# Kernel tuning notes

Hardware: AMD Instinct MI355X
Metric: run time of the kernel (lower is better)

## Reference

```python
import jax, jax.numpy as jnp
import numpy as np


def _ln(x, g, b, eps=1e-5):
    m = x.mean(-1, keepdims=True)
    v = x.var(-1, keepdims=True)
    return (x - m) / jnp.sqrt(v + eps) * g + b


def setup_inputs() -> dict:
    key = jax.random.key(0)
    ks = iter(jax.random.split(key, 48))
    B, N, H, Ld, L, FF = 2048, 10, 256, 8, 4, 1024
    def w(shape, s=0.02):
        return jax.random.normal(next(ks), shape, jnp.float32) * s
    return dict(
        latent_code=jax.random.normal(next(ks), (B, Ld), jnp.float32),
        target_node_types=jax.random.randint(next(ks), (B, N), 0, 5),
        ce_w1=w((Ld, H)), ce_b1=jnp.zeros(H), ce_g1=jnp.ones(H), ce_be1=jnp.zeros(H),
        ce_w2=w((H, H)), ce_b2=jnp.zeros(H), ce_g2=jnp.ones(H), ce_be2=jnp.zeros(H),
        nc_w1=w((2, H // 4)), nc_b1=jnp.zeros(H // 4), nc_w2=w((H // 4, 3)), nc_b2=jnp.zeros(3),
        type_emb=w((5, H), 1.0), pos_emb=w((N, H), 0.02),
        qkvo_w=w((L, 4, H, H)), qkvo_b=jnp.zeros((L, 4, H)),
        ln_g=jnp.ones((L, 2, H)), ln_b=jnp.zeros((L, 2, H)),
        ffn_w1=w((L, H, FF)), ffn_b1=jnp.zeros((L, FF)),
        ffn_w2=w((L, FF, H)), ffn_b2=jnp.zeros((L, H)),
        out_w=w((H, 5)), out_b=jnp.zeros(5),
        edge_w1=w((2 * H + Ld, H)), edge_b1=jnp.zeros(H),
        edge_w2=w((H, 8)), edge_b2=jnp.zeros(8),
    )


def reference(latent_code, target_node_types,
              ce_w1, ce_b1, ce_g1, ce_be1, ce_w2, ce_b2, ce_g2, ce_be2,
              nc_w1, nc_b1, nc_w2, nc_b2,
              type_emb, pos_emb, qkvo_w, qkvo_b, ln_g, ln_b,
              ffn_w1, ffn_b1, ffn_w2, ffn_b2, out_w, out_b,
              edge_w1, edge_b1, edge_w2, edge_b2):
    B, Ld = latent_code.shape
    N = target_node_types.shape[1]
    H = ce_w1.shape[1]
    L = qkvo_w.shape[0]
    nh = 8
    hd = H // nh

    # context encoder: Linear -> LN -> ReLU -> Linear -> LN
    h0 = jax.nn.relu(_ln(latent_code @ ce_w1 + ce_b1, ce_g1, ce_be1))
    context = _ln(h0 @ ce_w2 + ce_b2, ce_g2, ce_be2)  # [B,H]

    # node count head on latent_code[:, :2]
    node_count_logits = jax.nn.relu(latent_code[:, :2] @ nc_w1 + nc_b1) @ nc_w2 + nc_b2  # [B,3]

    # teacher-forced node embeddings (independent of predictions -> vectorizable)
    ne = type_emb[target_node_types] + pos_emb[:N]          # [B,N,H]
    h = context[:, None, :] + pos_emb[:N]                   # queries [B,N,H]
    mem = jnp.concatenate([context[:, None, :], ne], axis=1)  # keys [B,N+1,H]
    # position i attends to context (k=0) and nodes j<i (k=j+1), i.e. k <= i
    kmask = (jnp.arange(N + 1)[None, :] <= jnp.arange(N)[:, None])  # [N,N+1]
    scale = 1.0 / np.sqrt(hd).astype(np.float32)

    for l in range(L):
        Q = (h @ qkvo_w[l, 0] + qkvo_b[l, 0]).reshape(B, N, nh, hd)
        K = (mem @ qkvo_w[l, 1] + qkvo_b[l, 1]).reshape(B, N + 1, nh, hd)
        V = (mem @ qkvo_w[l, 2] + qkvo_b[l, 2]).reshape(B, N + 1, nh, hd)
        s = jnp.einsum('bnhd,bmhd->bhnm', Q, K) * scale
        s = jnp.where(kmask[None, None], s, jnp.float32(-1e9))
        a = jax.nn.softmax(s, axis=-1)
        o = jnp.einsum('bhnm,bmhd->bnhd', a, V).reshape(B, N, H)
        h = _ln(h + o @ qkvo_w[l, 3] + qkvo_b[l, 3], ln_g[l, 0], ln_b[l, 0])
        f = jax.nn.relu(h @ ffn_w1[l] + ffn_b1[l]) @ ffn_w2[l] + ffn_b2[l]
        h = _ln(h + f, ln_g[l, 1], ln_b[l, 1])

    node_logits = h @ out_w + out_b  # [B,N,5]

    # pairwise edge decoder on (emb_i, emb_j, latent) for i>j, symmetrized
    ei = jnp.broadcast_to(ne[:, :, None, :], (B, N, N, H))
    ej = jnp.broadcast_to(ne[:, None, :, :], (B, N, N, H))
    lat = jnp.broadcast_to(latent_code[:, None, None, :], (B, N, N, Ld))
    feat = jnp.concatenate([ei, ej, lat], axis=-1)  # [B,N,N,2H+Ld]
    elog = jax.nn.relu(feat @ edge_w1 + edge_b1) @ edge_w2 + edge_b2  # [B,N,N,8]
    tril = (jnp.arange(N)[:, None] > jnp.arange(N)[None, :])[None, :, :, None]
    lower = jnp.where(tril, elog, jnp.float32(0.0))
    edge_component_logits = lower + jnp.swapaxes(lower, 1, 2)  # diag stays zero

    return node_logits, node_count_logits, edge_component_logits
```

## Files before the change

kernel.cpp:

```cpp
#include <hip/hip_runtime.h>
#include <hip/hip_bf16.h>

#define BATCH 2048
#define NNODE 10
#define NLAYER 4
#define ROWS_H (BATCH*NNODE)
#define ROWS_M (BATCH*(NNODE+1))

typedef __hip_bfloat16 bf16;
typedef unsigned short u16;
typedef unsigned int u32;
typedef __attribute__((ext_vector_type(8))) short bf16x8;
typedef __attribute__((ext_vector_type(4))) float f32x4;

__device__ __forceinline__ float bfb(u16 u) {
    union { u32 i; float f; } c; c.i = (u32)u << 16; return c.f;
}
__device__ __forceinline__ float bf2f(bf16 x) { return __bfloat162float(x); }
__device__ __forceinline__ bf16 f2bf(float x) { return __float2bfloat16(x); }
__device__ __forceinline__ u16 f2u(float v) {
    bf16 t = f2bf(v); u16 u; __builtin_memcpy(&u, &t, 2); return u;
}
__device__ __forceinline__ void store_out(void* out, int f32o, size_t idx, float v) {
    if (f32o) ((float*)out)[idx] = v; else ((bf16*)out)[idx] = f2bf(v);
}
__device__ __forceinline__ int dflag(const u32* g) { return g[0] == 0x3F800000u; }

#define NT 26
struct CvtArgs { const void* src[NT]; int n[NT]; int off[NT]; };

__global__ __launch_bounds__(256) void cvt_kernel(CvtArgs a, bf16* __restrict__ dst,
                                                  const u32* __restrict__ gptr) {
    int f = dflag(gptr);
    int gid = blockIdx.x * 256 + threadIdx.x;
    int stride = gridDim.x * 256;
    for (int tn = 0; tn < NT; tn++) {
        const void* s = a.src[tn];
        bf16* d = dst + a.off[tn];
        int n = a.n[tn];
        if (f) {
            const float* sf = (const float*)s;
            for (int i = gid; i < n; i += stride) d[i] = f2bf(sf[i]);
        } else {
            const bf16* sb = (const bf16*)s;
            for (int i = gid; i < n; i += stride) d[i] = sb[i];
        }
    }
}

#define NTT 26
struct TTArgs { const void* src[NTT]; int soff[NTT]; int doff[NTT]; int R[NTT]; int Cc[NTT]; };

__global__ __launch_bounds__(256) void tt_kernel(TTArgs a, u16* __restrict__ dst,
                                                 const u32* __restrict__ gptr) {
    int f = dflag(gptr);
    int gid = blockIdx.x * 256 + threadIdx.x;
    int stride = gridDim.x * 256;
    for (int tn = 0; tn < NTT; tn++) {
        int R = a.R[tn], C = a.Cc[tn], n = R * C;
        u16* d = dst + a.doff[tn];
        if (f) {
            const float* s = (const float*)a.src[tn] + a.soff[tn];
            for (int i = gid; i < n; i += stride) {
                int r = i / C, c = i - r * C;
                d[c * R + r] = f2u(s[i]);
            }
        } else {
            const u16* s = (const u16*)a.src[tn] + a.soff[tn];
            for (int i = gid; i < n; i += stride) {
                int r = i / C, c = i - r * C;
                d[c * R + r] = s[i];
            }
        }
    }
}

__device__ __forceinline__ void ln_stats256(float x, float* s_red, float& m, float& var) {
    float v1 = x, v2 = x * x;
    #pragma unroll
    for (int off = 32; off; off >>= 1) {
        v1 += __shfl_down(v1, off, 64);
        v2 += __shfl_down(v2, off, 64);
    }
    int wave = threadIdx.x >> 6, lane = threadIdx.x & 63;
    if (!lane) { s_red[wave] = v1; s_red[4 + wave] = v2; }
    __syncthreads();
    m   = (s_red[0] + s_red[1] + s_red[2] + s_red[3]) * (1.f / 256.f);
    var = (s_red[4] + s_red[5] + s_red[6] + s_red[7]) * (1.f / 256.f) - m * m;
    __syncthreads();
}

__global__ __launch_bounds__(256) void ctx_kernel(
    const bf16* __restrict__ lat_bf, const int* __restrict__ types,
    const bf16* __restrict__ ce_w1, const bf16* __restrict__ ce_b1,
    const bf16* __restrict__ ce_g1, const bf16* __restrict__ ce_be1,
    const bf16* __restrict__ ce_w2, const bf16* __restrict__ ce_b2,
    const bf16* __restrict__ ce_g2, const bf16* __restrict__ ce_be2,
    const bf16* __restrict__ nc_w1, const bf16* __restrict__ nc_b1,
    const bf16* __restrict__ nc_w2, const bf16* __restrict__ nc_b2,
    const bf16* __restrict__ type_emb, const bf16* __restrict__ pos_emb,
    const bf16* __restrict__ edge_w1, const bf16* __restrict__ edge_b1,
    bf16* __restrict__ h, bf16* __restrict__ mem, bf16* __restrict__ ne,
    bf16* __restrict__ rvec, void* __restrict__ out, const u32* __restrict__ gptr)
{
    int b = blockIdx.x;
    int t = threadIdx.x;
    int f32o = dflag(gptr);
    __shared__ float lat[8];
    __shared__ float s_h0[256];
    __shared__ float s_red[8];
    __shared__ float s_nc[64];

    if (t < 8) lat[t] = bf2f(lat_bf[b * 8 + t]);
    __syncthreads();

    float x = bf2f(ce_b1[t]);
    #pragma unroll
    for (int k = 0; k < 8; k++) x += lat[k] * bf2f(ce_w1[k * 256 + t]);
    float m, var;
    ln_stats256(x, s_red, m, var);
    float r = rsqrtf(var + 1e-5f);
    float h0 = fmaxf((x - m) * r * bf2f(ce_g1[t]) + bf2f(ce_be1[t]), 0.f);
    s_h0[t] = h0;
    __syncthreads();

    float x2 = bf2f(ce_b2[t]);
    for (int k = 0; k < 256; k++) x2 += s_h0[k] * bf2f(ce_w2[k * 256 + t]);
    ln_stats256(x2, s_red, m, var);
    r = rsqrtf(var + 1e-5f);
    float ctx = (x2 - m) * r * bf2f(ce_g2[t]) + bf2f(ce_be2[t]);

    mem[(size_t)(b * 11) * 256 + t] = f2bf(ctx);
    for (int n = 0; n < NNODE; n++) {
        float pe = bf2f(pos_emb[n * 256 + t]);
        h[(size_t)(b * NNODE + n) * 256 + t] = f2bf(ctx + pe);
        int ty = types[b * NNODE + n];
        float nv = bf2f(type_emb[ty * 256 + t]) + pe;
        ne[(size_t)(b * NNODE + n) * 256 + t] = f2bf(nv);
        mem[(size_t)(b * 11 + 1 + n) * 256 + t] = f2bf(nv);
    }

    float rv = bf2f(edge_b1[t]);
    #pragma unroll
    for (int k = 0; k < 8; k++) rv += lat[k] * bf2f(edge_w1[(512 + k) * 256 + t]);
    rvec[(size_t)b * 256 + t] = f2bf(rv);

    if (t < 64) {
        float hn = lat[0] * bf2f(nc_w1[t]) + lat[1] * bf2f(nc_w1[64 + t]) + bf2f(nc_b1[t]);
        s_nc[t] = fmaxf(hn, 0.f);
    }
    __syncthreads();
    if (t < 3) {
        float o = bf2f(nc_b2[t]);
        for (int k = 0; k < 64; k++) o += s_nc[k] * bf2f(nc_w2[k * 3 + t]);
        store_out(out, f32o, (size_t)102400 + b * 3 + t, o);
    }
}

__global__ __launch_bounds__(256) void gemm_mfma(
    const u16* __restrict__ A, const u16* __restrict__ Bt,
    const bf16* __restrict__ bias, bf16* __restrict__ C,
    int M, int K, int N, int act)
{
    __shared__ u16 Als[128 * 32];
    __shared__ u16 Bls[128 * 32];
    int t = threadIdx.x;
    int w = t >> 6, l = t & 63;
    int m0 = blockIdx.y * 128, n0 = blockIdx.x * 128;
    int wr = (w >> 1) * 64, wc = (w & 1) * 64;

    int srow = w * 32 + (l >> 2);
    int selem = (l & 3) * 8;
    const u16* Ag = A + (size_t)(m0 + srow) * K + selem;
    const u16* Bg = Bt + (size_t)(n0 + srow) * K + selem;

    f32x4 acc[4][4];
    #pragma unroll
    for (int i = 0; i < 4; i++)
        #pragma unroll
        for (int j = 0; j < 4; j++)
            acc[i][j] = (f32x4){0.f, 0.f, 0.f, 0.f};

    int koff = (l >> 4) * 8;
    int mrow = wr + (l & 15);
    int ncol = wc + (l & 15);

    for (int kt = 0; kt < K; kt += 32) {
        const u16* ag = Ag + kt;
        const u16* bg = Bg + kt;
        __builtin_amdgcn_global_load_lds(
            (const __attribute__((address_space(1))) void*)ag,
            (__attribute__((address_space(3))) void*)&Als[w * 1024], 16, 0, 0);
        __builtin_amdgcn_global_load_lds(
            (const __attribute__((address_space(1))) void*)(ag + (size_t)16 * K),
            (__attribute__((address_space(3))) void*)&Als[w * 1024 + 512], 16, 0, 0);
        __builtin_amdgcn_global_load_lds(
            (const __attribute__((address_space(1))) void*)bg,
            (__attribute__((address_space(3))) void*)&Bls[w * 1024], 16, 0, 0);
        __builtin_amdgcn_global_load_lds(
            (const __attribute__((address_space(1))) void*)(bg + (size_t)16 * K),
            (__attribute__((address_space(3))) void*)&Bls[w * 1024 + 512], 16, 0, 0);
        __syncthreads();

        bf16x8 af[4], bfr[4];
        #pragma unroll
        for (int i = 0; i < 4; i++) {
            af[i]  = *(const bf16x8*)&Als[(mrow + i * 16) * 32 + koff];
            bfr[i] = *(const bf16x8*)&Bls[(ncol + i * 16) * 32 + koff];
        }
        #pragma unroll
        for (int i = 0; i < 4; i++)
            #pragma unroll
            for (int j = 0; j < 4; j++)
                acc[i][j] = __builtin_amdgcn_mfma_f32_16x16x32_bf16(af[i], bfr[j], acc[i][j], 0, 0, 0);
        __syncthreads();
    }

    int rbase = (l >> 4) * 4;
    #pragma unroll
    for (int i = 0; i < 4; i++) {
        int m = m0 + wr + i * 16 + rbase;
        #pragma unroll
        for (int j = 0; j < 4; j++) {
            int n = n0 + wc + j * 16 + (l & 15);
            float bv = bias ? bf2f(bias[n]) : 0.f;
            #pragma unroll
            for (int r = 0; r < 4; r++) {
                float v = acc[i][j][r] + bv;
                if (act) v = fmaxf(v, 0.f);
                C[(size_t)(m + r) * N + n] = f2bf(v);
            }
        }
    }
}

template<int MODE>
__global__ __launch_bounds__(256) void gemm_row(
    const u16* __restrict__ A, const u16* __restrict__ Bt,
    const bf16* __restrict__ bias, const bf16* __restrict__ g,
    const bf16* __restrict__ be, u16* __restrict__ hio,
    u16* __restrict__ C, int M, int K)
{
    __shared__ u16 Als[64 * 32];
    __shared__ u16 Bls[256 * 32];
    __shared__ float s_bias[256], s_g[256], s_be[256];
    int t = threadIdx.x;
    int w = t >> 6, l = t & 63;
    int m0 = blockIdx.x * 64;

    s_bias[t] = bf2f(bias[t]);
    if (MODE == 1) { s_g[t] = bf2f(g[t]); s_be[t] = bf2f(be[t]); }

    int srow = l >> 2, selem = (l & 3) * 8;
    const u16* Ag = A + (size_t)(m0 + w * 16 + srow) * K + selem;
    const u16* Bg = Bt + (size_t)(w * 64 + srow) * K + selem;

    f32x4 acc[16];
    #pragma unroll
    for (int j = 0; j < 16; j++) acc[j] = (f32x4){0.f, 0.f, 0.f, 0.f};

    int koff = (l >> 4) * 8;
    int l15 = l & 15;

    for (int kt = 0; kt < K; kt += 32) {
        __builtin_amdgcn_global_load_lds(
            (const __attribute__((address_space(1))) void*)(Ag + kt),
            (__attribute__((address_space(3))) void*)&Als[w * 512], 16, 0, 0);
        #pragma unroll
        for (int s = 0; s < 4; s++) {
            __builtin_amdgcn_global_load_lds(
                (const __attribute__((address_space(1))) void*)(Bg + kt + (size_t)(s * 16) * K),
                (__attribute__((address_space(3))) void*)&Bls[w * 2048 + s * 512], 16, 0, 0);
        }
        __syncthreads();

        bf16x8 af = *(const bf16x8*)&Als[(w * 16 + l15) * 32 + koff];
        #pragma unroll
        for (int j = 0; j < 16; j++) {
            bf16x8 bf = *(const bf16x8*)&Bls[(j * 16 + l15) * 32 + koff];
            acc[j] = __builtin_amdgcn_mfma_f32_16x16x32_bf16(af, bf, acc[j], 0, 0, 0);
        }
        __syncthreads();
    }

    int q = l >> 4;
    #pragma unroll
    for (int r = 0; r < 4; r++) {
        int row = m0 + w * 16 + q * 4 + r;
        if (MODE == 0) {
            #pragma unroll
            for (int j = 0; j < 16; j++) {
                int col = j * 16 + l15;
                C[(size_t)row * 256 + col] = f2u(acc[j][r] + s_bias[col]);
            }
        } else {
            float xs[16];
            float s = 0.f, s2 = 0.f;
            #pragma unroll
            for (int j = 0; j < 16; j++) {
                int col = j * 16 + l15;
                float xv = acc[j][r] + s_bias[col] + bfb(hio[(size_t)row * 256 + col]);
                xs[j] = xv; s += xv; s2 += xv * xv;
            }
            #pragma unroll
            for (int off = 8; off; off >>= 1) {
                s  += __shfl_xor(s, off, 64);
                s2 += __shfl_xor(s2, off, 64);
            }
            float mean = s * (1.f / 256.f);
            float var = s2 * (1.f / 256.f) - mean * mean;
            float rstd = rsqrtf(var + 1e-5f);
            #pragma unroll
            for (int j = 0; j < 16; j++) {
                int col = j * 16 + l15;
                hio[(size_t)row * 256 + col] = f2u((xs[j] - mean) * rstd * s_g[col] + s_be[col]);
            }
        }
    }
}

__global__ __launch_bounds__(256) void attn_kernel(
    const bf16* __restrict__ Qb, const bf16* __restrict__ KVb,
    bf16* __restrict__ Ob)
{
    int b = blockIdx.x;
    int t = threadIdx.x;
    __shared__ float Qs[10 * 256];
    __shared__ float Ks[11 * 256];
    __shared__ float S[880];

    for (int i = 0; i < 10; i++) Qs[i * 256 + t] = bf2f(Qb[(size_t)(b * 10 + i) * 256 + t]);
    for (int k = 0; k < 11; k++) Ks[k * 256 + t] = bf2f(KVb[(size_t)(b * 11 + k) * 512 + t]);
    __syncthreads();

    const float scale = 0.17677669529663687f;
    for (int e = t; e < 880; e += 256) {
        int head = e / 110, rem = e % 110, i = rem / 11, k = rem % 11;
        if (k <= i) {
            const float* qp = &Qs[i * 256 + head * 32];
            const float* kp = &Ks[k * 256 + head * 32];
            float s = 0.f;
            #pragma unroll
            for (int d = 0; d < 32; d++) s += qp[d] * kp[d];
            S[e] = s * scale;
        }
    }
    __syncthreads();
    if (t < 80) {
        int head = t / 10, i = t % 10;
        float* row = &S[head * 110 + i * 11];
        float mx = -1e30f;
        for (int k = 0; k <= i; k++) mx = fmaxf(mx, row[k]);
        float sum = 0.f;
        for (int k = 0; k <= i; k++) { float e = __expf(row[k] - mx); row[k] = e; sum += e; }
        float inv = 1.f / sum;
        for (int k = 0; k <= i; k++) row[k] *= inv;
    }
    __syncthreads();

    int head = t >> 5;
    float o[10] = {0.f, 0.f, 0.f, 0.f, 0.f, 0.f, 0.f, 0.f, 0.f, 0.f};
    for (int k = 0; k < 11; k++) {
        float v = bf2f(KVb[(size_t)(b * 11 + k) * 512 + 256 + t]);
        for (int i = k; i < 10; i++) o[i] += S[head * 110 + i * 11 + k] * v;
    }
    for (int i = 0; i < 10; i++) Ob[(size_t)(b * 10 + i) * 256 + t] = f2bf(o[i]);
}

__global__ __launch_bounds__(256) void outhead_kernel(
    const bf16* __restrict__ h, const bf16* __restrict__ w,
    const bf16* __restrict__ b, void* __restrict__ out, const u32* __restrict__ gptr)
{
    int f32o = dflag(gptr);
    int wv = threadIdx.x >> 6, l = threadIdx.x & 63;
    size_t row = (size_t)blockIdx.x * 4 + wv;
    ushort4 hv = *(const ushort4*)((const u16*)h + row * 256 + l * 4);
    float x[4] = {bfb(hv.x), bfb(hv.y), bfb(hv.z), bfb(hv.w)};
    float a[5] = {0.f, 0.f, 0.f, 0.f, 0.f};
    #pragma unroll
    for (int c = 0; c < 4; c++) {
        #pragma unroll
        for (int o = 0; o < 5; o++) a[o] += x[c] * bf2f(w[(l * 4 + c) * 5 + o]);
    }
    #pragma unroll
    for (int off = 32; off; off >>= 1)
        #pragma unroll
        for (int o = 0; o < 5; o++) a[o] += __shfl_xor(a[o], off, 64);
    if (!l)
        #pragma unroll
        for (int o = 0; o < 5; o++)
            store_out(out, f32o, row * 5 + o, a[o] + bf2f(b[o]));
}

__global__ __launch_bounds__(256) void edge_kernel(
    const bf16* __restrict__ PQ, const bf16* __restrict__ rvec,
    const bf16* __restrict__ w2, const bf16* __restrict__ b2,
    void* __restrict__ out, const u32* __restrict__ gptr)
{
    int f32o = dflag(gptr);
    int t = threadIdx.x, w = t >> 6, l = t & 63;
    int b = blockIdx.x * 4 + w;
    const size_t ebase = 108544;

    __shared__ u16 Pl[4][10 * 260];
    __shared__ u16 Ql[4][10 * 260];
    __shared__ u16 Rl[4][256];
    __shared__ float Wl[256 * 8];

    const u16* pq = (const u16*)PQ + (size_t)b * 10 * 512;
    #pragma unroll
    for (int i = 0; i < 10; i++) {
        ushort4 pv = *(const ushort4*)(pq + i * 512 + l * 4);
        ushort4 qv = *(const ushort4*)(pq + i * 512 + 256 + l * 4);
        *(ushort4*)&Pl[w][i * 260 + l * 4] = pv;
        *(ushort4*)&Ql[w][i * 260 + l * 4] = qv;
    }
    *(ushort4*)&Rl[w][l * 4] = *(const ushort4*)((const u16*)rvec + (size_t)b * 256 + l * 4);
    {
        const u16* wp = (const u16*)w2 + t * 8;
        #pragma unroll
        for (int o = 0; o < 8; o++) Wl[t * 8 + o] = bfb(wp[o]);
    }
    __syncthreads();

    if (l >= 45 && l < 55) {
        int i = l - 45;
        size_t o0 = ebase + ((size_t)(b * 10 + i) * 10 + i) * 8;
        if (f32o) {
            float4 z = {0.f, 0.f, 0.f, 0.f};
            *(float4*)((float*)out + o0) = z;
            *(float4*)((float*)out + o0 + 4) = z;
        } else {
            uint4 z = {0u, 0u, 0u, 0u};
            *(uint4*)((u16*)out + o0) = z;
        }
    }
    if (l < 45) {
        int i = 1;
        while (i * (i + 1) / 2 <= l) i++;
        int j = l - i * (i - 1) / 2;
        float acc[8] = {0.f, 0.f, 0.f, 0.f, 0.f, 0.f, 0.f, 0.f};
        const u16* Pp = &Pl[w][i * 260];
        const u16* Qp = &Ql[w][j * 260];
        const u16* Rp = &Rl[w][0];
        for (int c = 0; c < 256; c += 4) {
            ushort4 pv = *(const ushort4*)(Pp + c);
            ushort4 qv = *(const ushort4*)(Qp + c);
            ushort4 rv = *(const ushort4*)(Rp + c);
            float hc[4];
            hc[0] = fmaxf(bfb(pv.x) + bfb(qv.x) + bfb(rv.x), 0.f);
            hc[1] = fmaxf(bfb(pv.y) + bfb(qv.y) + bfb(rv.y), 0.f);
            hc[2] = fmaxf(bfb(pv.z) + bfb(qv.z) + bfb(rv.z), 0.f);
            hc[3] = fmaxf(bfb(pv.w) + bfb(qv.w) + bfb(rv.w), 0.f);
            #pragma unroll
            for (int cc = 0; cc < 4; cc++) {
                const float* wp = &Wl[(c + cc) * 8];
                #pragma unroll
                for (int o = 0; o < 8; o++) acc[o] += hc[cc] * wp[o];
            }
        }
        float r8[8];
        #pragma unroll
        for (int o = 0; o < 8; o++) r8[o] = acc[o] + bf2f(b2[o]);
        size_t o0 = ebase + ((size_t)(b * 10 + i) * 10 + j) * 8;
        size_t o1 = ebase + ((size_t)(b * 10 + j) * 10 + i) * 8;
        if (f32o) {
            float4 v0 = {r8[0], r8[1], r8[2], r8[3]};
            float4 v1 = {r8[4], r8[5], r8[6], r8[7]};
            *(float4*)((float*)out + o0) = v0; *(float4*)((float*)out + o0 + 4) = v1;
            *(float4*)((float*)out + o1) = v0; *(float4*)((float*)out + o1 + 4) = v1;
        } else {
            uint4 pk;
            pk.x = (u32)f2u(r8[0]) | ((u32)f2u(r8[1]) << 16);
            pk.y = (u32)f2u(r8[2]) | ((u32)f2u(r8[3]) << 16);
            pk.z = (u32)f2u(r8[4]) | ((u32)f2u(r8[5]) << 16);
            pk.w = (u32)f2u(r8[6]) | ((u32)f2u(r8[7]) << 16);
            *(uint4*)((u16*)out + o0) = pk;
            *(uint4*)((u16*)out + o1) = pk;
        }
    }
}

extern "C" void kernel_launch(void* const* d_in, const int* in_sizes, int n_in,
                              void* d_out, int out_size, void* d_ws, size_t ws_size,
                              hipStream_t stream) {
    const int* types = (const int*)d_in[1];
    const u32* gptr = (const u32*)d_in[18];

    static const int kIdx[NT] = {0,2,3,4,5,6,7,8,9,10,11,12,13,14,15,17,18,19,21,23,24,25,26,27,28,29};
    static const int kSz[NT]  = {16384,2048,256,256,256,65536,256,256,256,128,64,192,3,1280,2560,
                                 4096,2048,2048,4096,1024,1280,5,133120,256,2048,8};
    bf16* wbf = (bf16*)d_ws;

    CvtArgs ca;
    const bf16* cv[30];
    int off = 0;
    for (int i = 0; i < NT; i++) {
        ca.src[i] = d_in[kIdx[i]];
        ca.n[i] = kSz[i];
        ca.off[i] = off;
        cv[kIdx[i]] = wbf + off;
        off = (off + kSz[i] + 7) & ~7;
    }

    size_t wtbase_e = ((size_t)off + 127) & ~(size_t)127;
    u16* wt = (u16*)wbf + wtbase_e;
    TTArgs ta;
    int tn = 0;
    for (int l = 0; l < NLAYER; l++) {
        int base = l * 786432;
        for (int z = 0; z < 4; z++) {
            static const int dz[4] = {0, 65536, 131072, 196608};
            ta.src[tn] = d_in[16]; ta.soff[tn] = (l * 4 + z) * 65536;
            ta.doff[tn] = base + dz[z]; ta.R[tn] = 256; ta.Cc[tn] = 256; tn++;
        }
        ta.src[tn] = d_in[20]; ta.soff[tn] = l * 262144; ta.doff[tn] = base + 262144; ta.R[tn] = 256;  ta.Cc[tn] = 1024; tn++;
        ta.src[tn] = d_in[22]; ta.soff[tn] = l * 262144; ta.doff[tn] = base + 524288; ta.R[tn] = 1024; ta.Cc[tn] = 256;  tn++;
    }
    ta.src[tn] = d_in[26]; ta.soff[tn] = 0;     ta.doff[tn] = 3145728;         ta.R[tn] = 256; ta.Cc[tn] = 256; tn++;
    ta.src[tn] = d_in[26]; ta.soff[tn] = 65536; ta.doff[tn] = 3145728 + 65536; ta.R[tn] = 256; ta.Cc[tn] = 256; tn++;

    size_t actbase_e = wtbase_e + 3276800 + 128;

    size_t EH = (size_t)ROWS_H * 256, EM = (size_t)ROWS_M * 256;
    bf16* p = (bf16*)wbf + actbase_e;
    bf16* h    = p; p += EH;
    bf16* mem  = p; p += EM;
    bf16* ne   = p; p += EH;
    bf16* rvec = p; p += (size_t)BATCH * 256;
    bf16* span = p;
    bf16* qbuf = span;
    bf16* kvbuf = qbuf + EH;
    bf16* obuf = kvbuf + (size_t)ROWS_M * 512;
    bf16* fbuf = span;
    bf16* pqbuf = span;

    cvt_kernel<<<256, 256, 0, stream>>>(ca, wbf, gptr);
    tt_kernel<<<512, 256, 0, stream>>>(ta, wt, gptr);

    ctx_kernel<<<BATCH, 256, 0, stream>>>(
        cv[0], types, cv[2], cv[3], cv[4], cv[5], cv[6], cv[7], cv[8], cv[9],
        cv[10], cv[11], cv[12], cv[13], cv[14], cv[15], cv[26], cv[27],
        h, mem, ne, rvec, d_out, gptr);

    for (int l = 0; l < NLAYER; l++) {
        const u16* qT  = wt + (size_t)l * 786432;
        const u16* kvT = qT + 65536;
        const u16* oT  = qT + 196608;
        const u16* f1T = qT + 262144;
        const u16* f2T = qT + 524288;
        const bf16* bq  = cv[17] + (size_t)(l * 4 + 0) * 256;
        const bf16* bkv = cv[17] + (size_t)(l * 4 + 1) * 256;
        const bf16* bo  = cv[17] + (size_t)(l * 4 + 3) * 256;
        const bf16* g1 = cv[18] + (size_t)(l * 2) * 256, *be1 = cv[19] + (size_t)(l * 2) * 256;
        const bf16* g2 = cv[18] + (size_t)(l * 2 + 1) * 256, *be2 = cv[19] + (size_t)(l * 2 + 1) * 256;

        gemm_row<0><<<ROWS_H / 64, 256, 0, stream>>>((const u16*)h, qT, bq, nullptr, nullptr,
                                                     nullptr, (u16*)qbuf, ROWS_H, 256);
        gemm_mfma<<<dim3(4, ROWS_M / 128), 256, 0, stream>>>((const u16*)mem, kvT, bkv, kvbuf, ROWS_M, 256, 512, 0);
        attn_kernel<<<BATCH, 256, 0, stream>>>(qbuf, kvbuf, obuf);
        gemm_row<1><<<ROWS_H / 64, 256, 0, stream>>>((const u16*)obuf, oT, bo, g1, be1,
                                                     (u16*)h, nullptr, ROWS_H, 256);
        gemm_mfma<<<dim3(8, ROWS_H / 128), 256, 0, stream>>>((const u16*)h, f1T, cv[21] + (size_t)l * 1024, fbuf, ROWS_H, 256, 1024, 1);
        gemm_row<1><<<ROWS_H / 64, 256, 0, stream>>>((const u16*)fbuf, f2T, cv[23] + (size_t)l * 256, g2, be2,
                                                     (u16*)h, nullptr, ROWS_H, 1024);
    }

    outhead_kernel<<<ROWS_H / 4, 256, 0, stream>>>(h, cv[24], cv[25], d_out, gptr);

    gemm_mfma<<<dim3(4, ROWS_H / 128), 256, 0, stream>>>((const u16*)ne, wt + 3145728, nullptr, pqbuf, ROWS_H, 256, 512, 0);
    edge_kernel<<<BATCH / 4, 256, 0, stream>>>(pqbuf, rvec, cv[28], cv[29], d_out, gptr);
}
```

Baseline: 743.2 us.

## Fuse FFN up/down projections into one kernel and retile row GEMMs

Replaces the separate FFN up-projection GEMM and down-projection+LayerNorm GEMM with a single kernel. Each 64-row block keeps its input rows and the ReLU intermediate in LDS, streaming 128-column chunks of the hidden layer so the 1024-wide intermediate never goes to global memory. It also retiles the 256-column row GEMM so each wave owns a 64-column slice across all 64 rows, with LayerNorm statistics reduced across waves through shared memory. The cost is more LDS per block, lower occupancy, and the FFN loops run serially inside one block with many syncs.

Result: no change. 738.9 us (-0.6%).

```diff
diff --git a/kernel.cpp b/kernel.cpp
--- a/kernel.cpp
+++ b/kernel.cpp
@@ -25,6 +25,10 @@
     if (f32o) ((float*)out)[idx] = v; else ((bf16*)out)[idx] = f2bf(v);
 }
 __device__ __forceinline__ int dflag(const u32* g) { return g[0] == 0x3F800000u; }
+
+#define GLL(src, dst) __builtin_amdgcn_global_load_lds( \
+    (const __attribute__((address_space(1))) void*)(src), \
+    (__attribute__((address_space(3))) void*)(dst), 16, 0, 0)
 
 #define NT 26
 struct CvtArgs { const void* src[NT]; int n[NT]; int off[NT]; };
@@ -188,18 +192,10 @@
     for (int kt = 0; kt < K; kt += 32) {
         const u16* ag = Ag + kt;
         const u16* bg = Bg + kt;
-        __builtin_amdgcn_global_load_lds(
-            (const __attribute__((address_space(1))) void*)ag,
-            (__attribute__((address_space(3))) void*)&Als[w * 1024], 16, 0, 0);
-        __builtin_amdgcn_global_load_lds(
-            (const __attribute__((address_space(1))) void*)(ag + (size_t)16 * K),
-            (__attribute__((address_space(3))) void*)&Als[w * 1024 + 512], 16, 0, 0);
-        __builtin_amdgcn_global_load_lds(
-            (const __attribute__((address_space(1))) void*)bg,
-            (__attribute__((address_space(3))) void*)&Bls[w * 1024], 16, 0, 0);
-        __builtin_amdgcn_global_load_lds(
-            (const __attribute__((address_space(1))) void*)(bg + (size_t)16 * K),
-            (__attribute__((address_space(3))) void*)&Bls[w * 1024 + 512], 16, 0, 0);
+        GLL(ag, &Als[w * 1024]);
+        GLL(ag + (size_t)16 * K, &Als[w * 1024 + 512]);
+        GLL(bg, &Bls[w * 1024]);
+        GLL(bg + (size_t)16 * K, &Bls[w * 1024 + 512]);
         __syncthreads();
 
         bf16x8 af[4], bfr[4];
@@ -235,88 +231,241 @@
 }
 
 template<int MODE>
-__global__ __launch_bounds__(256) void gemm_row(
+__global__ __launch_bounds__(256) void gemm256(
     const u16* __restrict__ A, const u16* __restrict__ Bt,
     const bf16* __restrict__ bias, const bf16* __restrict__ g,
     const bf16* __restrict__ be, u16* __restrict__ hio,
-    u16* __restrict__ C, int M, int K)
+    u16* __restrict__ C, int K)
 {
-    __shared__ u16 Als[64 * 32];
-    __shared__ u16 Bls[256 * 32];
-    __shared__ float s_bias[256], s_g[256], s_be[256];
-    int t = threadIdx.x;
-    int w = t >> 6, l = t & 63;
+    __shared__ u16 Asl[64 * 32];
+    __shared__ u16 Bsl[256 * 32];
+    __shared__ float lnp[2][4][64];
+    int t = threadIdx.x, w = t >> 6, l = t & 63, q = l >> 4, l15 = l & 15;
     int m0 = blockIdx.x * 64;
 
-    s_bias[t] = bf2f(bias[t]);
-    if (MODE == 1) { s_g[t] = bf2f(g[t]); s_be[t] = bf2f(be[t]); }
-
-    int srow = l >> 2, selem = (l & 3) * 8;
-    const u16* Ag = A + (size_t)(m0 + w * 16 + srow) * K + selem;
-    const u16* Bg = Bt + (size_t)(w * 64 + srow) * K + selem;
-
-    f32x4 acc[16];
-    #pragma unroll
-    for (int j = 0; j < 16; j++) acc[j] = (f32x4){0.f, 0.f, 0.f, 0.f};
-
-    int koff = (l >> 4) * 8;
-    int l15 = l & 15;
+    const u16* Ag = A + (size_t)(m0 + w * 16 + (l >> 2)) * K + (l & 3) * 8;
+    const u16* Bg = Bt + (size_t)(w * 64 + (l >> 2)) * K + (l & 3) * 8;
+
+    f32x4 acc[4][4];
+    #pragma unroll
+    for (int i = 0; i < 4; i++)
+        #pragma unroll
+        for (int j = 0; j < 4; j++)
+            acc[i][j] = (f32x4){0.f, 0.f, 0.f, 0.f};
 
     for (int kt = 0; kt < K; kt += 32) {
-        __builtin_amdgcn_global_load_lds(
-            (const __attribute__((address_space(1))) void*)(Ag + kt),
-            (__attribute__((address_space(3))) void*)&Als[w * 512], 16, 0, 0);
-        #pragma unroll
-        for (int s = 0; s < 4; s++) {
-            __builtin_amdgcn_global_load_lds(
-                (const __attribute__((address_space(1))) void*)(Bg + kt + (size_t)(s * 16) * K),
-                (__attribute__((address_space(3))) void*)&Bls[w * 2048 + s * 512], 16, 0, 0);
-        }
+        GLL(Ag + kt, &Asl[w * 512]);
+        #pragma unroll
+        for (int s = 0; s < 4; s++)
+            GLL(Bg + kt + (size_t)(s * 16) * K, &Bsl[w * 2048 + s * 512]);
         __syncthreads();
-
-        bf16x8 af = *(const bf16x8*)&Als[(w * 16 + l15) * 32 + koff];
-        #pragma unroll
-        for (int j = 0; j < 16; j++) {
-            bf16x8 bf = *(const bf16x8*)&Bls[(j * 16 + l15) * 32 + koff];
-            acc[j] = __builtin_amdgcn_mfma_f32_16x16x32_bf16(af, bf, acc[j], 0, 0, 0);
-        }
+        bf16x8 af[4], bfr[4];
+        #pragma unroll
+        for (int i = 0; i < 4; i++)
+            af[i] = *(const bf16x8*)&Asl[(i * 16 + l15) * 32 + q * 8];
+        #pragma unroll
+        for (int j = 0; j < 4; j++)
+            bfr[j] = *(const bf16x8*)&Bsl[(w * 64 + j * 16 + l15) * 32 + q * 8];
+        #pragma unroll
+        for (int i = 0; i < 4; i++)
+            #pragma unroll
+            for (int j = 0; j < 4; j++)
+                acc[i][j] = __builtin_amdgcn_mfma_f32_16x16x32_bf16(af[i], bfr[j], acc[i][j], 0, 0, 0);
         __syncthreads();
     }
 
-    int q = l >> 4;
-    #pragma unroll
-    for (int r = 0; r < 4; r++) {
-        int row = m0 + w * 16 + q * 4 + r;
-        if (MODE == 0) {
-            #pragma unroll
-            for (int j = 0; j < 16; j++) {
-                int col = j * 16 + l15;
-                C[(size_t)row * 256 + col] = f2u(acc[j][r] + s_bias[col]);
-            }
-        } else {
-            float xs[16];
+    float bv[4];
+    #pragma unroll
+    for (int j = 0; j < 4; j++) bv[j] = bf2f(bias[w * 64 + j * 16 + l15]);
+
+    if (MODE == 0) {
+        #pragma unroll
+        for (int i = 0; i < 4; i++)
+            #pragma unroll
+            for (int r = 0; r < 4; r++) {
+                int row = m0 + i * 16 + q * 4 + r;
+                #pragma unroll
+                for (int j = 0; j < 4; j++)
+                    C[(size_t)row * 256 + w * 64 + j * 16 + l15] = f2u(acc[i][j][r] + bv[j]);
+            }
+    } else {
+        float gv[4], bev[4];
+        #pragma unroll
+        for (int j = 0; j < 4; j++) {
+            gv[j] = bf2f(g[w * 64 + j * 16 + l15]);
+            bev[j] = bf2f(be[w * 64 + j * 16 + l15]);
+        }
+        #pragma unroll
+        for (int i = 0; i < 4; i++)
+            #pragma unroll
+            for (int r = 0; r < 4; r++) {
+                int row = m0 + i * 16 + q * 4 + r;
+                float s = 0.f, s2 = 0.f;
+                #pragma unroll
+                for (int j = 0; j < 4; j++) {
+                    float xv = acc[i][j][r] + bv[j] + bfb(hio[(size_t)row * 256 + w * 64 + j * 16 + l15]);
+                    acc[i][j][r] = xv; s += xv; s2 += xv * xv;
+                }
+                #pragma unroll
+                for (int d = 1; d < 16; d <<= 1) {
+                    s  += __shfl_xor(s, d, 64);
+                    s2 += __shfl_xor(s2, d, 64);
+                }
+                if (l15 == 0) {
+                    lnp[0][w][i * 16 + q * 4 + r] = s;
+                    lnp[1][w][i * 16 + q * 4 + r] = s2;
+                }
+            }
+        __syncthreads();
+        #pragma unroll
+        for (int i = 0; i < 4; i++)
+            #pragma unroll
+            for (int r = 0; r < 4; r++) {
+                int lr = i * 16 + q * 4 + r;
+                float S  = lnp[0][0][lr] + lnp[0][1][lr] + lnp[0][2][lr] + lnp[0][3][lr];
+                float S2 = lnp[1][0][lr] + lnp[1][1][lr] + lnp[1][2][lr] + lnp[1][3][lr];
+                float mean = S * (1.f / 256.f);
+                float var = S2 * (1.f / 256.f) - mean * mean;
+                float rstd = rsqrtf(var + 1e-5f);
+                #pragma unroll
+                for (int j = 0; j < 4; j++)
+                    hio[(size_t)(m0 + lr) * 256 + w * 64 + j * 16 + l15] =
+                        f2u((acc[i][j][r] - mean) * rstd * gv[j] + bev[j]);
+            }
+    }
+}
+
+__global__ __launch_bounds__(256) void ffn_kernel(
+    u16* __restrict__ h, const u16* __restrict__ W1T, const u16* __restrict__ W2T,
+    const bf16* __restrict__ b1, const bf16* __restrict__ b2,
+    const bf16* __restrict__ g, const bf16* __restrict__ be)
+{
+    __shared__ u16 Asl[64 * 264];
+    __shared__ u16 W1s[128 * 32];
+    __shared__ u16 mids[64 * 136];
+    __shared__ u16 W2s[256 * 32];
+    __shared__ float lnp[2][4][64];
+
+    int t = threadIdx.x, w = t >> 6, l = t & 63, q = l >> 4, l15 = l & 15;
+    int m0 = blockIdx.x * 64;
+
+    {
+        int row = t >> 2, seg = (t & 3) * 64;
+        const u16* src = h + (size_t)(m0 + row) * 256 + seg;
+        u16* dst = &Asl[row * 264 + seg];
+        #pragma unroll
+        for (int u = 0; u < 8; u++)
+            *(uint4*)(dst + u * 8) = *(const uint4*)(src + u * 8);
+    }
+
+    f32x4 accO[4][4];
+    #pragma unroll
+    for (int i = 0; i < 4; i++)
+        #pragma unroll
+        for (int j = 0; j < 4; j++)
+            accO[i][j] = (f32x4){0.f, 0.f, 0.f, 0.f};
+    __syncthreads();
+
+    for (int c = 0; c < 8; c++) {
+        f32x4 accM[4][2];
+        #pragma unroll
+        for (int i = 0; i < 4; i++) { accM[i][0] = (f32x4){0,0,0,0}; accM[i][1] = (f32x4){0,0,0,0}; }
+
+        for (int kt = 0; kt < 256; kt += 32) {
+            const u16* src = W1T + (size_t)(c * 128 + w * 32 + (l >> 2)) * 256 + kt + (l & 3) * 8;
+            GLL(src, &W1s[w * 1024]);
+            GLL(src + (size_t)16 * 256, &W1s[w * 1024 + 512]);
+            __syncthreads();
+            bf16x8 af[4], bfm[2];
+            #pragma unroll
+            for (int i = 0; i < 4; i++)
+                af[i] = *(const bf16x8*)&Asl[(i * 16 + l15) * 264 + kt + q * 8];
+            #pragma unroll
+            for (int j = 0; j < 2; j++)
+                bfm[j] = *(const bf16x8*)&W1s[(w * 32 + j * 16 + l15) * 32 + q * 8];
+            #pragma unroll
+            for (int i = 0; i < 4; i++)
+                #pragma unroll
+                for (int j = 0; j < 2; j++)
+                    accM[i][j] = __builtin_amdgcn_mfma_f32_16x16x32_bf16(af[i], bfm[j], accM[i][j], 0, 0, 0);
+            __syncthreads();
+        }
+        float b1v[2];
+        #pragma unroll
+        for (int j = 0; j < 2; j++) b1v[j] = bf2f(b1[c * 128 + w * 32 + j * 16 + l15]);
+        #pragma unroll
+        for (int i = 0; i < 4; i++)
+            #pragma unroll
+            for (int j = 0; j < 2; j++)
+                #pragma unroll
+                for (int r = 0; r < 4; r++) {
+                    int row = i * 16 + q * 4 + r, col = w * 32 + j * 16 + l15;
+                    mids[row * 136 + col] = f2u(fmaxf(accM[i][j][r] + b1v[j], 0.f));
+                }
+        __syncthreads();
+
+        for (int kt2 = 0; kt2 < 4; kt2++) {
+            const u16* src = W2T + (size_t)(w * 64 + (l >> 2)) * 1024 + c * 128 + kt2 * 32 + (l & 3) * 8;
+            #pragma unroll
+            for (int s = 0; s < 4; s++)
+                GLL(src + (size_t)(s * 16) * 1024, &W2s[w * 2048 + s * 512]);
+            __syncthreads();
+            bf16x8 am[4], bo[4];
+            #pragma unroll
+            for (int i = 0; i < 4; i++)
+                am[i] = *(const bf16x8*)&mids[(i * 16 + l15) * 136 + kt2 * 32 + q * 8];
+            #pragma unroll
+            for (int j = 0; j < 4; j++)
+                bo[j] = *(const bf16x8*)&W2s[(w * 64 + j * 16 + l15) * 32 + q * 8];
+            #pragma unroll
+            for (int i = 0; i < 4; i++)
+                #pragma unroll
+                for (int j = 0; j < 4; j++)
+                    accO[i][j] = __builtin_amdgcn_mfma_f32_16x16x32_bf16(am[i], bo[j], accO[i][j], 0, 0, 0);
+            __syncthreads();
+        }
+    }
+
+    float b2v[4], gv[4], bev[4];
+    #pragma unroll
+    for (int j = 0; j < 4; j++) {
+        int col = w * 64 + j * 16 + l15;
+        b2v[j] = bf2f(b2[col]); gv[j] = bf2f(g[col]); bev[j] = bf2f(be[col]);
+    }
+    #pragma unroll
+    for (int i = 0; i < 4; i++)
+        #pragma unroll
+        for (int r = 0; r < 4; r++) {
+            int row = i * 16 + q * 4 + r;
             float s = 0.f, s2 = 0.f;
             #pragma unroll
-            for (int j = 0; j < 16; j++) {
-                int col = j * 16 + l15;
-                float xv = acc[j][r] + s_bias[col] + bfb(hio[(size_t)row * 256 + col]);
-                xs[j] = xv; s += xv; s2 += xv * xv;
-            }
-            #pragma unroll
-            for (int off = 8; off; off >>= 1) {
-                s  += __shfl_xor(s, off, 64);
-                s2 += __shfl_xor(s2, off, 64);
-            }
-            float mean = s * (1.f / 256.f);
-            float var = s2 * (1.f / 256.f) - mean * mean;
+            for (int j = 0; j < 4; j++) {
+                float xv = accO[i][j][r] + b2v[j] + bfb(Asl[row * 264 + w * 64 + j * 16 + l15]);
+                accO[i][j][r] = xv; s += xv; s2 += xv * xv;
+            }
+            #pragma unroll
+            for (int d = 1; d < 16; d <<= 1) {
+                s  += __shfl_xor(s, d, 64);
+                s2 += __shfl_xor(s2, d, 64);
+            }
+            if (l15 == 0) { lnp[0][w][row] = s; lnp[1][w][row] = s2; }
+        }
+    __syncthreads();
+    #pragma unroll
+    for (int i = 0; i < 4; i++)
+        #pragma unroll
+        for (int r = 0; r < 4; r++) {
+            int lr = i * 16 + q * 4 + r;
+            float S  = lnp[0][0][lr] + lnp[0][1][lr] + lnp[0][2][lr] + lnp[0][3][lr];
+            float S2 = lnp[1][0][lr] + lnp[1][1][lr] + lnp[1][2][lr] + lnp[1][3][lr];
+            float mean = S * (1.f / 256.f);
+            float var = S2 * (1.f / 256.f) - mean * mean;
             float rstd = rsqrtf(var + 1e-5f);
             #pragma unroll
-            for (int j = 0; j < 16; j++) {
-                int col = j * 16 + l15;
-                hio[(size_t)row * 256 + col] = f2u((xs[j] - mean) * rstd * s_g[col] + s_be[col]);
-            }
-        }
-    }
+            for (int j = 0; j < 4; j++)
+                h[(size_t)(m0 + lr) * 256 + w * 64 + j * 16 + l15] =
+                    f2u((accO[i][j][r] - mean) * rstd * gv[j] + bev[j]);
+        }
 }
 
 __global__ __launch_bounds__(256) void attn_kernel(
@@ -532,7 +681,6 @@
     bf16* qbuf = span;
     bf16* kvbuf = qbuf + EH;
     bf16* obuf = kvbuf + (size_t)ROWS_M * 512;
-    bf16* fbuf = span;
     bf16* pqbuf = span;
 
     cvt_kernel<<<256, 256, 0, stream>>>(ca, wbf, gptr);
@@ -555,15 +703,15 @@
         const bf16* g1 = cv[18] + (size_t)(l * 2) * 256, *be1 = cv[19] + (size_t)(l * 2) * 256;
         const bf16* g2 = cv[18] + (size_t)(l * 2 + 1) * 256, *be2 = cv[19] + (size_t)(l * 2 + 1) * 256;
 
-        gemm_row<0><<<ROWS_H / 64, 256, 0, stream>>>((const u16*)h, qT, bq, nullptr, nullptr,
-                                                     nullptr, (u16*)qbuf, ROWS_H, 256);
+        gemm256<0><<<ROWS_H / 64, 256, 0, stream>>>((const u16*)h, qT, bq, nullptr, nullptr,
+                                                    nullptr, (u16*)qbuf, 256);
         gemm_mfma<<<dim3(4, ROWS_M / 128), 256, 0, stream>>>((const u16*)mem, kvT, bkv, kvbuf, ROWS_M, 256, 512, 0);
         attn_kernel<<<BATCH, 256, 0, stream>>>(qbuf, kvbuf, obuf);
-        gemm_row<1><<<ROWS_H / 64, 256, 0, stream>>>((const u16*)obuf, oT, bo, g1, be1,
-                                                     (u16*)h, nullptr, ROWS_H, 256);
-        gemm_mfma<<<dim3(8, ROWS_H / 128), 256, 0, stream>>>((const u16*)h, f1T, cv[21] + (size_t)l * 1024, fbuf, ROWS_H, 256, 1024, 1);
-        gemm_row<1><<<ROWS_H / 64, 256, 0, stream>>>((const u16*)fbuf, f2T, cv[23] + (size_t)l * 256, g2, be2,
-                                                     (u16*)h, nullptr, ROWS_H, 1024);
+        gemm256<1><<<ROWS_H / 64, 256, 0, stream>>>((const u16*)obuf, oT, bo, g1, be1,
+                                                    (u16*)h, nullptr, 256);
+        ffn_kernel<<<ROWS_H / 64, 256, 0, stream>>>((u16*)h, f1T, f2T,
+                                                    cv[21] + (size_t)l * 1024, cv[23] + (size_t)l * 256,
+                                                    g2, be2);
     }
 
     outhead_kernel<<<ROWS_H / 4, 256, 0, stream>>>(h, cv[24], cv[25], d_out, gptr);
```
